# Optimization experiments

Hardware: AMD Instinct MI355X
Metric: run time of the kernel (lower is better)

The kernel has to match this reference:

```python
import jax, jax.numpy as jnp
import numpy as np

THR = 1.0
ALPHA = 5.0
C = 0.4
TAU_U = 20.0
DT = 1.0

def slayer(x):
    # SE-adlif SLAYER surrogate: c*alpha / (2*exp(alpha*|x|))
    return C * ALPHA / (2.0 * jnp.exp(jnp.abs(x) * ALPHA))

def setup_inputs() -> dict:
    key = jax.random.key(0)
    k1, k2, k3 = jax.random.split(key, 3)
    B, T, IN, OUT = 64, 1000, 512, 512
    x = jax.random.normal(k1, (B, T, IN), dtype=jnp.float32)
    lim = 1.0 / np.sqrt(IN)
    weight = jax.random.uniform(k2, (OUT, IN), minval=-lim, maxval=lim, dtype=jnp.float32)
    bias = jnp.zeros((OUT,), jnp.float32)
    # orthogonal init for recurrent weights
    recurrent = jnp.linalg.qr(jax.random.normal(k3, (OUT, OUT), dtype=jnp.float32))[0].astype(jnp.float32)
    # fixed tau trainer: decay = exp(-dt/tau)
    decay = jnp.full((OUT,), np.exp(-DT / TAU_U), dtype=jnp.float32)
    return {"input_tensor": x, "weight": weight, "bias": bias, "recurrent": recurrent, "decay": decay}

def reference(input_tensor, weight, bias, recurrent, decay):
    B = input_tensor.shape[0]
    OUT = weight.shape[0]
    sg = jax.lax.stop_gradient
    # precompute input-driven current for all timesteps: [B, T, OUT]
    cur = jnp.einsum('bti,oi->bto', input_tensor, weight) + bias
    v0 = jnp.zeros((B, OUT), jnp.float32)
    z0 = jnp.zeros((B, OUT), jnp.float32)

    def step(carry, c_t):
        v_tm1, z_tm1 = carry
        v_tm1 = v_tm1 * (1.0 - sg(z_tm1))  # detached reset
        soma = c_t + z_tm1 @ recurrent.T
        v_t = decay * v_tm1 + (1.0 - decay) * soma
        v_thr = v_t - THR
        hv = jnp.where(v_thr >= 0, 1.0, 0.0).astype(v_thr.dtype)
        # straight-through: value = heaviside, grad = SLAYER surrogate
        z_t = sg(hv) + (v_thr - sg(v_thr)) * sg(slayer(v_thr))
        return (v_t, z_t), (v_t, z_t)

    _, (vs, zs) = jax.lax.scan(step, (v0, z0), jnp.swapaxes(cur, 0, 1))
    vs = jnp.swapaxes(vs, 0, 1)  # [B, T, OUT]
    zs = jnp.swapaxes(zs, 0, 1)
    v_full = jnp.concatenate([v0[:, None], vs], axis=1)  # [B, T+1, OUT]
    z_full = jnp.concatenate([z0[:, None], zs], axis=1)
    states = jnp.stack([v_full, z_full], axis=0)  # [2, B, T+1, OUT]
    outputs = zs  # [B, T, OUT]
    return outputs, states
```

## Files before the change

kernel.cpp:

```cpp
#include <hip/hip_runtime.h>

#define SV_OFF 32768000
#define SZ_OFF 65568768

typedef __attribute__((ext_vector_type(8))) short bf16x8;
typedef __attribute__((ext_vector_type(4))) float f32x4;

__device__ __forceinline__ unsigned short f2bf(float f) {
  union { float f; unsigned u; } x; x.f = f;
  unsigned r = x.u + 0x7fffu + ((x.u >> 16) & 1u);
  return (unsigned short)(r >> 16);
}

__device__ __forceinline__ void gl_lds16(const void* g, void* l) {
  __builtin_amdgcn_global_load_lds(
      (const __attribute__((address_space(1))) unsigned int*)g,
      (__attribute__((address_space(3))) unsigned int*)l, 16, 0, 0);
}

__global__ __launch_bounds__(256) void prep(const float* __restrict__ W,
                                            unsigned short* __restrict__ Wb,
                                            int* __restrict__ flags) {
  const int idx = blockIdx.x * 256 + threadIdx.x;
  if (idx < 512 * 512) Wb[idx] = f2bf(W[idx]);
  if (idx < 64) flags[idx] = 0;
}

__global__ __launch_bounds__(256) void cvt_x(const float* __restrict__ x,
                                             unsigned short* __restrict__ xb) {
  const size_t i = ((size_t)blockIdx.x * 256 + threadIdx.x) * 8;
  const float4 a = *(const float4*)(x + i);
  const float4 b = *(const float4*)(x + i + 4);
  bf16x8 h;
  h[0] = (short)f2bf(a.x); h[1] = (short)f2bf(a.y);
  h[2] = (short)f2bf(a.z); h[3] = (short)f2bf(a.w);
  h[4] = (short)f2bf(b.x); h[5] = (short)f2bf(b.y);
  h[6] = (short)f2bf(b.z); h[7] = (short)f2bf(b.w);
  *(bf16x8*)(xb + i) = h;
}

__global__ __launch_bounds__(320, 2) void fused(
    const unsigned short* __restrict__ Ab,
    const unsigned short* __restrict__ Wb,
    const float* __restrict__ bias,
    const float* __restrict__ decay,
    float* __restrict__ out,
    int* __restrict__ flags) {
  __shared__ unsigned short As[4][128][32];
  __shared__ unsigned short Bs[4][64][32];
  __shared__ float cs[128][64];

  const int b    = blockIdx.x;
  const int o0   = blockIdx.y * 64;
  const int tid  = threadIdx.x;
  const int lane = tid & 63;
  const int wave = tid >> 6;
  const int lr = lane & 15;
  const int lq = lane >> 4;
  const int wr = wave >> 1;
  const int wc = wave & 1;

  const int row0 = tid >> 2;
  const int scol = ((tid & 3) * 16) ^ ((row0 & 3) << 4);
  const char* abase = (const char*)Ab + (size_t)b * 1000 * 1024;
  const char* bbase = (const char*)Wb + (size_t)o0 * 1024;

#define STAGE(s_) do {                                                          \
    const int t0_ = ((s_) >> 4) * 128;                                          \
    const int kb_ = ((s_) & 15) * 64;                                           \
    const int bf_ = (s_) & 3;                                                   \
    gl_lds16(abase + (size_t)(t0_ + row0) * 1024 + kb_ + scol,                  \
             (char*)&As[bf_][0][0] + tid * 16);                                 \
    gl_lds16(abase + (size_t)(t0_ + 64 + row0) * 1024 + kb_ + scol,             \
             (char*)&As[bf_][0][0] + tid * 16 + 4096);                          \
    gl_lds16(bbase + (size_t)row0 * 1024 + kb_ + scol,                          \
             (char*)&Bs[bf_][0][0] + tid * 16);                                 \
  } while (0)

  float v = 0.f, d = 0.f, om = 0.f, bv = 0.f;
  int fl = 0;
  if (tid >= 256) {
    const int o = tid - 256;
    d  = decay[o0 + o];
    om = 1.f - d;
    bv = bias[o0 + o];
    __builtin_nontemporal_store(0.f, out + SV_OFF + (size_t)b * 512512 + o0 + o);
    __builtin_nontemporal_store(0.f, out + SZ_OFF + (size_t)b * 512512 + o0 + o);
  } else {
    STAGE(0); STAGE(1); STAGE(2);
  }

  int s = 0;
  for (int tile = 0; tile < 8; ++tile) {
    f32x4 acc[4][2] = {};
    for (int kk = 0; kk < 16; ++kk, ++s) {
      if (tid < 256)
        asm volatile("s_waitcnt vmcnt(6)" ::: "memory");
      __builtin_amdgcn_s_barrier();
      __builtin_amdgcn_sched_barrier(0);
      if (tid < 256) {
        if (s < 125) STAGE(s + 3);
        const int bf_ = s & 3;
        const int fo = (lq ^ (lr & 3)) * 8;
        bf16x8 af[4], bq[2];
#pragma unroll
        for (int i = 0; i < 4; ++i)
          af[i] = *(const bf16x8*)(&As[bf_][wr * 64 + i * 16 + lr][fo]);
#pragma unroll
        for (int j = 0; j < 2; ++j)
          bq[j] = *(const bf16x8*)(&Bs[bf_][wc * 32 + j * 16 + lr][fo]);
#pragma unroll
        for (int i = 0; i < 4; ++i)
#pragma unroll
          for (int j = 0; j < 2; ++j)
            acc[i][j] = __builtin_amdgcn_mfma_f32_16x16x32_bf16(af[i], bq[j], acc[i][j], 0, 0, 0);
      } else if (tile > 0) {
        const int o = tid - 256;
        const int pt0 = (tile - 1) * 128;
        const int tb = kk * 8;
        float* zp = out + ((size_t)b * 1000 + pt0) * 512 + o0 + o;
        float* vp = out + SV_OFF + ((size_t)b * 1001 + pt0 + 1) * 512 + o0 + o;
        float* sp = out + SZ_OFF + ((size_t)b * 1001 + pt0 + 1) * 512 + o0 + o;
#pragma unroll
        for (int u = 0; u < 8; ++u) {
          const int t = tb + u;
          const float c = cs[t][o ^ (((t >> 2) & 1) << 4)];
          v = d * v + om * (c + bv);
          const float z = (v >= 1.0f) ? 1.0f : 0.0f;
          fl |= (v >= 1.0f);
          __builtin_nontemporal_store(z, zp + (size_t)t * 512);
          __builtin_nontemporal_store(v, vp + (size_t)t * 512);
          __builtin_nontemporal_store(z, sp + (size_t)t * 512);
        }
      }
    }
    __builtin_amdgcn_s_barrier();
    __builtin_amdgcn_sched_barrier(0);
    if (tid < 256) {
#pragma unroll
      for (int i = 0; i < 4; ++i)
#pragma unroll
        for (int j = 0; j < 2; ++j) {
          const int tb = wr * 64 + i * 16 + lq * 4;
          const int cc = (wc * 32 + j * 16 + lr) ^ ((lq & 1) << 4);
#pragma unroll
          for (int r = 0; r < 4; ++r) cs[tb + r][cc] = acc[i][j][r];
        }
      asm volatile("s_waitcnt lgkmcnt(0)" ::: "memory");
    }
    __builtin_amdgcn_s_barrier();
    __builtin_amdgcn_sched_barrier(0);
  }
  if (tid >= 256) {
    const int o = tid - 256;
    const int pt0 = 896;
    float* zp = out + ((size_t)b * 1000 + pt0) * 512 + o0 + o;
    float* vp = out + SV_OFF + ((size_t)b * 1001 + pt0 + 1) * 512 + o0 + o;
    float* sp = out + SZ_OFF + ((size_t)b * 1001 + pt0 + 1) * 512 + o0 + o;
    for (int t = 0; t < 104; ++t) {
      const float c = cs[t][o ^ (((t >> 2) & 1) << 4)];
      v = d * v + om * (c + bv);
      const float z = (v >= 1.0f) ? 1.0f : 0.0f;
      fl |= (v >= 1.0f);
      __builtin_nontemporal_store(z, zp + (size_t)t * 512);
      __builtin_nontemporal_store(v, vp + (size_t)t * 512);
      __builtin_nontemporal_store(z, sp + (size_t)t * 512);
    }
    if (fl) atomicOr(flags + b, 1);
  }
#undef STAGE
}

__global__ __launch_bounds__(512) void scan_fix(const float* __restrict__ x,
                                                const float* __restrict__ W,
                                                const float* __restrict__ bias,
                                                const float* __restrict__ R,
                                                const float* __restrict__ decay,
                                                float* __restrict__ out,
                                                const int* __restrict__ flags) {
  const int b = blockIdx.x;
  if (flags[b] == 0) return;
  const int o = threadIdx.x;
  __shared__ float xs[512];
  __shared__ int cnt;
  __shared__ int list[512];
  const float d = decay[o];
  const float om = 1.f - d;
  float v = 0.f, z = 0.f;
  const size_t zb  = (size_t)b * 512000 + o;
  const size_t svb = (size_t)b * 512512 + o;
  float* __restrict__ sv = out + SV_OFF;
  float* __restrict__ sz = out + SZ_OFF;
  sv[svb] = 0.f;
  sz[svb] = 0.f;
  if (o == 0) cnt = 0;
  __syncthreads();
  for (int t = 0; t < 1000; ++t) {
    xs[o] = x[((size_t)b * 1000 + t) * 512 + o];
    __syncthreads();
    float soma = bias[o];
    for (int i = 0; i < 512; ++i) soma += xs[i] * W[(size_t)o * 512 + i];
    const int n = cnt;
    for (int i = 0; i < n; ++i) soma += R[(size_t)o * 512 + list[i]];
    v = d * (v * (1.f - z)) + om * soma;
    z = (v >= 1.0f) ? 1.0f : 0.0f;
    out[zb + (size_t)t * 512] = z;
    sv[svb + (size_t)(t + 1) * 512] = v;
    sz[svb + (size_t)(t + 1) * 512] = z;
    __syncthreads();
    if (o == 0) cnt = 0;
    __syncthreads();
    if (z != 0.f) { const int q = atomicAdd(&cnt, 1); list[q] = o; }
    __syncthreads();
  }
}

extern "C" void kernel_launch(void* const* d_in, const int* in_sizes, int n_in,
                              void* d_out, int out_size, void* d_ws, size_t ws_size,
                              hipStream_t stream) {
  (void)in_sizes; (void)n_in; (void)out_size; (void)ws_size;
  const float* x     = (const float*)d_in[0];
  const float* W     = (const float*)d_in[1];
  const float* bias  = (const float*)d_in[2];
  const float* R     = (const float*)d_in[3];
  const float* decay = (const float*)d_in[4];
  float* out = (float*)d_out;

  char* ws = (char*)d_ws;
  unsigned short* xb = (unsigned short*)ws;
  unsigned short* Wb = (unsigned short*)(ws + 65536000);
  int* flags         = (int*)(ws + 66060288);

  prep<<<1024, 256, 0, stream>>>(W, Wb, flags);
  cvt_x<<<16000, 256, 0, stream>>>(x, xb);
  fused<<<dim3(64, 8), 320, 0, stream>>>(xb, Wb, bias, decay, out, flags);
  scan_fix<<<64, 512, 0, stream>>>(x, W, bias, R, decay, out, flags);
}
```

Baseline: 584.6 us.

## Widen fused GEMM tile to 128 outputs with 8 compute waves

Each fused block now covers 128 output columns instead of 64, using 8 MFMA waves plus 2 scan waves (640 threads, one block per CU). Grid shrinks from 64x8 to 64x4, so each input tile is loaded once for twice as many outputs, halving redundant A reads. Also wraps MFMA issue in s_setprio, always issues the prefetch stage with a wrapped index, and widens the LDS swizzle. Risks: lower occupancy, larger LDS use, and only 256 blocks for the device's CUs, which can leave CUs idle.

```diff
diff --git a/kernel.cpp b/kernel.cpp
--- a/kernel.cpp
+++ b/kernel.cpp
@@ -39,7 +39,7 @@
   *(bf16x8*)(xb + i) = h;
 }
 
-__global__ __launch_bounds__(320, 2) void fused(
+__global__ __launch_bounds__(640, 1) void fused(
     const unsigned short* __restrict__ Ab,
     const unsigned short* __restrict__ Wb,
     const float* __restrict__ bias,
@@ -47,18 +47,19 @@
     float* __restrict__ out,
     int* __restrict__ flags) {
   __shared__ unsigned short As[4][128][32];
-  __shared__ unsigned short Bs[4][64][32];
-  __shared__ float cs[128][64];
+  __shared__ unsigned short Bs[4][128][32];
+  __shared__ float cs[128][128];
 
   const int b    = blockIdx.x;
-  const int o0   = blockIdx.y * 64;
+  const int o0   = blockIdx.y * 128;
   const int tid  = threadIdx.x;
   const int lane = tid & 63;
   const int wave = tid >> 6;
+  const bool gemm = tid < 512;
   const int lr = lane & 15;
   const int lq = lane >> 4;
-  const int wr = wave >> 1;
-  const int wc = wave & 1;
+  const int wr = (wave >> 2) & 1;
+  const int wc = wave & 3;
 
   const int row0 = tid >> 2;
   const int scol = ((tid & 3) * 16) ^ ((row0 & 3) << 4);
@@ -71,21 +72,19 @@
     const int bf_ = (s_) & 3;                                                   \
     gl_lds16(abase + (size_t)(t0_ + row0) * 1024 + kb_ + scol,                  \
              (char*)&As[bf_][0][0] + tid * 16);                                 \
-    gl_lds16(abase + (size_t)(t0_ + 64 + row0) * 1024 + kb_ + scol,             \
-             (char*)&As[bf_][0][0] + tid * 16 + 4096);                          \
     gl_lds16(bbase + (size_t)row0 * 1024 + kb_ + scol,                          \
              (char*)&Bs[bf_][0][0] + tid * 16);                                 \
   } while (0)
 
+  const int so = tid - 512;
   float v = 0.f, d = 0.f, om = 0.f, bv = 0.f;
   int fl = 0;
-  if (tid >= 256) {
-    const int o = tid - 256;
-    d  = decay[o0 + o];
+  if (!gemm) {
+    d  = decay[o0 + so];
     om = 1.f - d;
-    bv = bias[o0 + o];
-    __builtin_nontemporal_store(0.f, out + SV_OFF + (size_t)b * 512512 + o0 + o);
-    __builtin_nontemporal_store(0.f, out + SZ_OFF + (size_t)b * 512512 + o0 + o);
+    bv = bias[o0 + so];
+    __builtin_nontemporal_store(0.f, out + SV_OFF + (size_t)b * 512512 + o0 + so);
+    __builtin_nontemporal_store(0.f, out + SZ_OFF + (size_t)b * 512512 + o0 + so);
   } else {
     STAGE(0); STAGE(1); STAGE(2);
   }
@@ -94,12 +93,12 @@
   for (int tile = 0; tile < 8; ++tile) {
     f32x4 acc[4][2] = {};
     for (int kk = 0; kk < 16; ++kk, ++s) {
-      if (tid < 256)
-        asm volatile("s_waitcnt vmcnt(6)" ::: "memory");
+      if (gemm)
+        asm volatile("s_waitcnt vmcnt(4)" ::: "memory");
       __builtin_amdgcn_s_barrier();
       __builtin_amdgcn_sched_barrier(0);
-      if (tid < 256) {
-        if (s < 125) STAGE(s + 3);
+      if (gemm) {
+        STAGE((s + 3) & 127);
         const int bf_ = s & 3;
         const int fo = (lq ^ (lr & 3)) * 8;
         bf16x8 af[4], bq[2];
@@ -109,40 +108,41 @@
 #pragma unroll
         for (int j = 0; j < 2; ++j)
           bq[j] = *(const bf16x8*)(&Bs[bf_][wc * 32 + j * 16 + lr][fo]);
+        __builtin_amdgcn_s_setprio(1);
 #pragma unroll
         for (int i = 0; i < 4; ++i)
 #pragma unroll
           for (int j = 0; j < 2; ++j)
             acc[i][j] = __builtin_amdgcn_mfma_f32_16x16x32_bf16(af[i], bq[j], acc[i][j], 0, 0, 0);
+        __builtin_amdgcn_s_setprio(0);
       } else if (tile > 0) {
-        const int o = tid - 256;
         const int pt0 = (tile - 1) * 128;
         const int tb = kk * 8;
-        float* zp = out + ((size_t)b * 1000 + pt0) * 512 + o0 + o;
-        float* vp = out + SV_OFF + ((size_t)b * 1001 + pt0 + 1) * 512 + o0 + o;
-        float* sp = out + SZ_OFF + ((size_t)b * 1001 + pt0 + 1) * 512 + o0 + o;
+        float* zp = out + ((size_t)b * 1000 + pt0 + tb) * 512 + o0 + so;
+        float* vp = out + SV_OFF + ((size_t)b * 1001 + pt0 + tb + 1) * 512 + o0 + so;
+        float* sp = out + SZ_OFF + ((size_t)b * 1001 + pt0 + tb + 1) * 512 + o0 + so;
 #pragma unroll
         for (int u = 0; u < 8; ++u) {
           const int t = tb + u;
-          const float c = cs[t][o ^ (((t >> 2) & 1) << 4)];
+          const float c = cs[t][so ^ (((t >> 2) & 3) << 4)];
           v = d * v + om * (c + bv);
           const float z = (v >= 1.0f) ? 1.0f : 0.0f;
           fl |= (v >= 1.0f);
-          __builtin_nontemporal_store(z, zp + (size_t)t * 512);
-          __builtin_nontemporal_store(v, vp + (size_t)t * 512);
-          __builtin_nontemporal_store(z, sp + (size_t)t * 512);
+          __builtin_nontemporal_store(z, zp + (size_t)u * 512);
+          __builtin_nontemporal_store(v, vp + (size_t)u * 512);
+          __builtin_nontemporal_store(z, sp + (size_t)u * 512);
         }
       }
     }
     __builtin_amdgcn_s_barrier();
     __builtin_amdgcn_sched_barrier(0);
-    if (tid < 256) {
+    if (gemm) {
 #pragma unroll
       for (int i = 0; i < 4; ++i)
 #pragma unroll
         for (int j = 0; j < 2; ++j) {
           const int tb = wr * 64 + i * 16 + lq * 4;
-          const int cc = (wc * 32 + j * 16 + lr) ^ ((lq & 1) << 4);
+          const int cc = (wc * 32 + j * 16 + lr) ^ (lq << 4);
 #pragma unroll
           for (int r = 0; r < 4; ++r) cs[tb + r][cc] = acc[i][j][r];
         }
@@ -151,14 +151,13 @@
     __builtin_amdgcn_s_barrier();
     __builtin_amdgcn_sched_barrier(0);
   }
-  if (tid >= 256) {
-    const int o = tid - 256;
+  if (!gemm) {
     const int pt0 = 896;
-    float* zp = out + ((size_t)b * 1000 + pt0) * 512 + o0 + o;
-    float* vp = out + SV_OFF + ((size_t)b * 1001 + pt0 + 1) * 512 + o0 + o;
-    float* sp = out + SZ_OFF + ((size_t)b * 1001 + pt0 + 1) * 512 + o0 + o;
+    float* zp = out + ((size_t)b * 1000 + pt0) * 512 + o0 + so;
+    float* vp = out + SV_OFF + ((size_t)b * 1001 + pt0 + 1) * 512 + o0 + so;
+    float* sp = out + SZ_OFF + ((size_t)b * 1001 + pt0 + 1) * 512 + o0 + so;
     for (int t = 0; t < 104; ++t) {
-      const float c = cs[t][o ^ (((t >> 2) & 1) << 4)];
+      const float c = cs[t][so ^ (((t >> 2) & 3) << 4)];
       v = d * v + om * (c + bv);
       const float z = (v >= 1.0f) ? 1.0f : 0.0f;
       fl |= (v >= 1.0f);
@@ -233,6 +232,6 @@
 
   prep<<<1024, 256, 0, stream>>>(W, Wb, flags);
   cvt_x<<<16000, 256, 0, stream>>>(x, xb);
-  fused<<<dim3(64, 8), 320, 0, stream>>>(xb, Wb, bias, decay, out, flags);
+  fused<<<dim3(64, 4), 640, 0, stream>>>(xb, Wb, bias, decay, out, flags);
   scan_fix<<<64, 512, 0, stream>>>(x, W, bias, R, decay, out, flags);
 }
```

After: 526.9 us. -9.9%, faster.
